# Kernel optimization log

Hardware: AMD Instinct MI355X
Metric: run time of the kernel (lower is better)

The kernel has to match this reference:

```python
import jax, jax.numpy as jnp
import numpy as np

HIDDEN = 1024
EMB = 256
VOCAB = 500000
B = 4096
C = 128
EPS = 1e-12


def setup_inputs() -> dict:
    key = jax.random.key(0)
    ks = jax.random.split(key, 8)
    hidden_states = jax.random.normal(ks[0], (B, HIDDEN), dtype=jnp.float32)
    cand_idx = jax.random.randint(ks[1], (B, C), 0, VOCAB, dtype=jnp.int32)
    W_dense = jax.random.normal(ks[2], (EMB, HIDDEN), dtype=jnp.float32) * (1.0 / np.sqrt(HIDDEN))
    b_dense = jnp.zeros((EMB,), dtype=jnp.float32)
    ln_gamma = jnp.ones((EMB,), dtype=jnp.float32)
    ln_beta = jnp.zeros((EMB,), dtype=jnp.float32)
    decoder_table = jax.random.normal(ks[3], (VOCAB, EMB), dtype=jnp.float32) * 0.02
    entity_bias = jnp.zeros((VOCAB,), dtype=jnp.float32)
    return {
        "hidden_states": hidden_states,
        "W_dense": W_dense,
        "b_dense": b_dense,
        "ln_gamma": ln_gamma,
        "ln_beta": ln_beta,
        "decoder_table": decoder_table,
        "entity_bias": entity_bias,
        "cand_idx": cand_idx,
    }


def _transform(x, W_dense, b_dense, ln_gamma, ln_beta):
    # Linear hidden_size -> entity_emb_size, gelu, LayerNorm
    h = x @ W_dense.T + b_dense
    h = jax.nn.gelu(h, approximate=False)
    mu = jnp.mean(h, axis=-1, keepdims=True)
    var = jnp.mean(jnp.square(h - mu), axis=-1, keepdims=True)
    return (h - mu) * jax.lax.rsqrt(var + EPS) * ln_gamma + ln_beta


def reference(hidden_states, W_dense, b_dense, ln_gamma, ln_beta, decoder_table, entity_bias, cand_idx):
    h = _transform(hidden_states, W_dense, b_dense, ln_gamma, ln_beta)  # [B, EMB]
    cand_emb = decoder_table[cand_idx]          # [B, C, EMB] ragged gather (padded)
    bias = entity_bias[cand_idx]                # [B, C]
    scores = jnp.einsum('bce,be->bc', cand_emb, h) + bias  # [B, C]
    return scores
```

## Files before the change

### kernel.cpp

```cpp
#include <hip/hip_runtime.h>
#include <hip/hip_bf16.h>
#include <math.h>

#define HIDDEN 1024
#define EMB    256
#define BROWS  4096
#define CAND   128
#define LN_EPS 1e-12f

typedef __attribute__((ext_vector_type(8))) short bf16x8;
typedef __attribute__((ext_vector_type(4))) float f32x4;

__device__ __forceinline__ int swz(int row, int slot) { return slot ^ ((row >> 1) & 3); }

__device__ __forceinline__ unsigned short f2bf(float f) {
    __bf16 h = (__bf16)f;
    return __builtin_bit_cast(unsigned short, h);
}

__device__ __forceinline__ float gelu(float x) {
    return 0.5f * x * (1.0f + erff(x * 0.70710678118654752f));
}

__global__ __launch_bounds__(256) void k_gemm_partial(
    const float* __restrict__ A,
    const float* __restrict__ W,
    float* __restrict__ P)
{
    __shared__ unsigned short As[16 * 32];
    __shared__ unsigned short Ws[256 * 32];

    const int tid  = threadIdx.x;
    const int lane = tid & 63;
    const int wv   = tid >> 6;
    const int m0   = blockIdx.x * 16;
    const int ks   = blockIdx.y;
    const int kbeg = ks * 256;

    const int lcol = lane & 15;
    const int lk   = lane >> 4;
    const int arow = tid >> 2, apr = tid & 3;

    float4 a0, a1, w0[4], w1[4];

#define LOADREGS(KT)                                                          \
    if (tid < 64) {                                                           \
        a0 = *(const float4*)&A[(size_t)(m0 + arow) * HIDDEN + (KT) + apr * 8];     \
        a1 = *(const float4*)&A[(size_t)(m0 + arow) * HIDDEN + (KT) + apr * 8 + 4]; \
    }                                                                         \
    _Pragma("unroll")                                                         \
    for (int i = 0; i < 4; ++i) {                                             \
        int id = tid + i * 256;                                               \
        int row = id >> 2, pr = id & 3;                                       \
        w0[i] = *(const float4*)&W[(size_t)row * HIDDEN + (KT) + pr * 8];     \
        w1[i] = *(const float4*)&W[(size_t)row * HIDDEN + (KT) + pr * 8 + 4]; \
    }

    f32x4 acc[4] = {};
    LOADREGS(kbeg)

    for (int it = 0; it < 8; ++it) {
        __syncthreads();
        if (tid < 64) {
            bf16x8 v;
            v[0]=f2bf(a0.x); v[1]=f2bf(a0.y); v[2]=f2bf(a0.z); v[3]=f2bf(a0.w);
            v[4]=f2bf(a1.x); v[5]=f2bf(a1.y); v[6]=f2bf(a1.z); v[7]=f2bf(a1.w);
            *(bf16x8*)&As[arow * 32 + swz(arow, apr) * 8] = v;
        }
        #pragma unroll
        for (int i = 0; i < 4; ++i) {
            int id = tid + i * 256;
            int row = id >> 2, pr = id & 3;
            bf16x8 v;
            v[0]=f2bf(w0[i].x); v[1]=f2bf(w0[i].y); v[2]=f2bf(w0[i].z); v[3]=f2bf(w0[i].w);
            v[4]=f2bf(w1[i].x); v[5]=f2bf(w1[i].y); v[6]=f2bf(w1[i].z); v[7]=f2bf(w1[i].w);
            *(bf16x8*)&Ws[row * 32 + swz(row, pr) * 8] = v;
        }
        __syncthreads();
        if (it < 7) { LOADREGS(kbeg + (it + 1) * 32) }
        bf16x8 af = *(const bf16x8*)&As[lcol * 32 + swz(lcol, lk) * 8];
        bf16x8 bfr[4];
        #pragma unroll
        for (int n = 0; n < 4; ++n) {
            int r = wv * 64 + n * 16 + lcol;
            bfr[n] = *(const bf16x8*)&Ws[r * 32 + swz(r, lk) * 8];
        }
        #pragma unroll
        for (int n = 0; n < 4; ++n)
            acc[n] = __builtin_amdgcn_mfma_f32_16x16x32_bf16(af, bfr[n], acc[n], 0, 0, 0);
    }
#undef LOADREGS

    float* Pout = P + (size_t)ks * ((size_t)BROWS * EMB);
    #pragma unroll
    for (int n = 0; n < 4; ++n)
        #pragma unroll
        for (int r = 0; r < 4; ++r) {
            int R   = lk * 4 + r;
            int col = wv * 64 + n * 16 + lcol;
            Pout[(size_t)(m0 + R) * EMB + col] = acc[n][r];
        }
}

__global__ __launch_bounds__(256) void k_finalize(
    const float* __restrict__ P,
    const float* __restrict__ bias,
    const float* __restrict__ gamma,
    const float* __restrict__ beta,
    float* __restrict__ G)
{
    const int tid  = threadIdx.x;
    const int lane = tid & 63;
    const int row  = blockIdx.x * 4 + (tid >> 6);
    const size_t off = (size_t)row * EMB + lane * 4;
    const size_t S   = (size_t)BROWS * EMB;

    float4 v0 = *(const float4*)&P[off];
    float4 v1 = *(const float4*)&P[off + S];
    float4 v2 = *(const float4*)&P[off + 2 * S];
    float4 v3 = *(const float4*)&P[off + 3 * S];
    float4 bb = *(const float4*)&bias[lane * 4];

    float4 h;
    h.x = gelu(v0.x + v1.x + v2.x + v3.x + bb.x);
    h.y = gelu(v0.y + v1.y + v2.y + v3.y + bb.y);
    h.z = gelu(v0.z + v1.z + v2.z + v3.z + bb.z);
    h.w = gelu(v0.w + v1.w + v2.w + v3.w + bb.w);

    float s = h.x + h.y + h.z + h.w;
    #pragma unroll
    for (int m = 32; m >= 1; m >>= 1) s += __shfl_xor(s, m);
    const float mu = s * (1.0f / 256.0f);

    const float dx = h.x - mu, dy = h.y - mu, dz = h.z - mu, dw = h.w - mu;
    float q = dx * dx + dy * dy + dz * dz + dw * dw;
    #pragma unroll
    for (int m = 32; m >= 1; m >>= 1) q += __shfl_xor(q, m);
    const float rs = rsqrtf(q * (1.0f / 256.0f) + LN_EPS);

    float4 g  = *(const float4*)&gamma[lane * 4];
    float4 be = *(const float4*)&beta[lane * 4];
    float4 o;
    o.x = dx * rs * g.x + be.x;
    o.y = dy * rs * g.y + be.y;
    o.z = dz * rs * g.z + be.z;
    o.w = dw * rs * g.w + be.w;
    *(float4*)&G[off] = o;
}

__global__ __launch_bounds__(256) void k_scores(
    const float* __restrict__ H,
    const float* __restrict__ table,
    const float* __restrict__ ebias,
    const int*   __restrict__ cidx,
    float* __restrict__ out)
{
    __shared__ float smem[16384];
    const int tid  = threadIdx.x;
    const int lane = tid & 63;
    const int wv   = tid >> 6;
    const int l    = lane & 15;
    const int q    = lane >> 4;
    const int b     = blockIdx.x >> 1;
    const int cbase = (blockIdx.x & 1) * 64 + wv * 16;

    const float4* Hrow = (const float4*)(H + (size_t)b * EMB);
    float4 hv[4];
    #pragma unroll
    for (int p = 0; p < 4; ++p) hv[p] = Hrow[p * 16 + l];

    const int sidxv = cidx[(size_t)b * CAND + cbase + l];
    const float ebv = ebias[sidxv];

    float* wbase = &smem[wv * 4096];
    #pragma unroll
    for (int r = 0; r < 16; ++r) {
        int idx = __shfl(sidxv, r);
        const float* gsrc = table + (size_t)idx * EMB + lane * 4;
        __builtin_amdgcn_global_load_lds(
            (const __attribute__((address_space(1))) void*)gsrc,
            (__attribute__((address_space(3))) void*)(wbase + r * 256),
            16, 0, 0);
    }

    float res[4];
#define DOGROUP(g, WN)                                                        \
    {                                                                         \
        asm volatile("s_waitcnt vmcnt(" WN ")" ::: "memory");                 \
        const float4* row = (const float4*)(wbase + (4 * (g) + q) * 256);     \
        float s = 0.f;                                                        \
        _Pragma("unroll")                                                     \
        for (int p = 0; p < 4; ++p) {                                         \
            float4 t = row[p * 16 + l];                                       \
            s += t.x * hv[p].x + t.y * hv[p].y + t.z * hv[p].z + t.w * hv[p].w;\
        }                                                                     \
        _Pragma("unroll")                                                     \
        for (int m = 8; m >= 1; m >>= 1) s += __shfl_xor(s, m);               \
        res[g] = s;                                                           \
    }
    DOGROUP(0, "12")
    DOGROUP(1, "8")
    DOGROUP(2, "4")
    DOGROUP(3, "0")
#undef DOGROUP

    #pragma unroll
    for (int g = 0; g < 4; ++g) {
        float eb = __shfl(ebv, 4 * g + q);
        if (l == 0) out[(size_t)b * CAND + cbase + 4 * g + q] = res[g] + eb;
    }
}

extern "C" void kernel_launch(void* const* d_in, const int* in_sizes, int n_in,
                              void* d_out, int out_size, void* d_ws, size_t ws_size,
                              hipStream_t stream) {
    const float* hidden = (const float*)d_in[0];
    const float* Wd     = (const float*)d_in[1];
    const float* bd     = (const float*)d_in[2];
    const float* gamma  = (const float*)d_in[3];
    const float* beta   = (const float*)d_in[4];
    const float* table  = (const float*)d_in[5];
    const float* ebias  = (const float*)d_in[6];
    const int*   cidx   = (const int*)d_in[7];
    float* out = (float*)d_out;

    char* ws = (char*)d_ws;
    float* G = (float*)ws;
    float* P = (float*)(ws + 4 * 1024 * 1024);

    k_gemm_partial<<<dim3(BROWS / 16, 4), 256, 0, stream>>>(hidden, Wd, P);
    k_finalize<<<dim3(BROWS / 4), 256, 0, stream>>>(P, bd, gamma, beta, G);
    k_scores<<<dim3(BROWS * 2), 256, 0, stream>>>(G, table, ebias, cidx, out);
}
```

Measured before the change: 119.7 us.

## Make scores kernel persistent with double-buffered LDS gather prefetch

The scores kernel previously launched one short-lived block per half row. It now launches 512 persistent blocks, and each wave walks 32 chunks of 8 candidates. While the current chunk is being computed, the wave prefetches the next chunk's table rows into a second LDS buffer, along with its H row, candidate indices and bias. The goal is to hide gather latency and remove per-block launch and prologue overhead. The cost is in-flight parallelism that is fixed by the grid size, plus more complex vmcnt bookkeeping.

```diff
diff --git a/kernel.cpp b/kernel.cpp
--- a/kernel.cpp
+++ b/kernel.cpp
@@ -7,6 +7,10 @@
 #define BROWS  4096
 #define CAND   128
 #define LN_EPS 1e-12f
+
+#define NC     8
+#define NWTOT  2048
+#define NITER  32
 
 typedef __attribute__((ext_vector_type(8))) short bf16x8;
 typedef __attribute__((ext_vector_type(4))) float f32x4;
@@ -149,7 +153,7 @@
 }
 
 __global__ __launch_bounds__(256) void k_scores(
-    const float* __restrict__ H,
+    const float* __restrict__ Hf,
     const float* __restrict__ table,
     const float* __restrict__ ebias,
     const int*   __restrict__ cidx,
@@ -161,54 +165,99 @@
     const int wv   = tid >> 6;
     const int l    = lane & 15;
     const int q    = lane >> 4;
-    const int b     = blockIdx.x >> 1;
-    const int cbase = (blockIdx.x & 1) * 64 + wv * 16;
-
-    const float4* Hrow = (const float4*)(H + (size_t)b * EMB);
-    float4 hv[4];
-    #pragma unroll
-    for (int p = 0; p < 4; ++p) hv[p] = Hrow[p * 16 + l];
-
-    const int sidxv = cidx[(size_t)b * CAND + cbase + l];
-    const float ebv = ebias[sidxv];
-
-    float* wbase = &smem[wv * 4096];
-    #pragma unroll
-    for (int r = 0; r < 16; ++r) {
-        int idx = __shfl(sidxv, r);
-        const float* gsrc = table + (size_t)idx * EMB + lane * 4;
+    const int w    = blockIdx.x * 4 + wv;
+
+    float* buf0 = &smem[wv * 4096];
+    float* buf1 = buf0 + 2048;
+
+#define CH(IT) ((((IT) < NITER) ? (IT) : (NITER - 1)) * NWTOT + w)
+
+    int ia = cidx[(size_t)CH(0) * NC + (l & 7)];
+    int ib = cidx[(size_t)CH(1) * NC + (l & 7)];
+    float4 ha[4];
+    {
+        const float4* Hr = (const float4*)(Hf + (size_t)(CH(0) >> 4) * EMB);
+        #pragma unroll
+        for (int p = 0; p < 4; ++p) ha[p] = Hr[p * 16 + l];
+    }
+    float ea = ebias[ia];
+    #pragma unroll
+    for (int r = 0; r < NC; ++r) {
+        int ix = __shfl(ia, r);
+        const float* gs = table + (size_t)ix * EMB + lane * 4;
         __builtin_amdgcn_global_load_lds(
-            (const __attribute__((address_space(1))) void*)gsrc,
-            (__attribute__((address_space(3))) void*)(wbase + r * 256),
+            (const __attribute__((address_space(1))) void*)gs,
+            (__attribute__((address_space(3))) void*)(buf0 + r * 256),
             16, 0, 0);
     }
 
-    float res[4];
-#define DOGROUP(g, WN)                                                        \
-    {                                                                         \
-        asm volatile("s_waitcnt vmcnt(" WN ")" ::: "memory");                 \
-        const float4* row = (const float4*)(wbase + (4 * (g) + q) * 256);     \
-        float s = 0.f;                                                        \
-        _Pragma("unroll")                                                     \
-        for (int p = 0; p < 4; ++p) {                                         \
-            float4 t = row[p * 16 + l];                                       \
-            s += t.x * hv[p].x + t.y * hv[p].y + t.z * hv[p].z + t.w * hv[p].w;\
-        }                                                                     \
-        _Pragma("unroll")                                                     \
-        for (int m = 8; m >= 1; m >>= 1) s += __shfl_xor(s, m);               \
-        res[g] = s;                                                           \
-    }
-    DOGROUP(0, "12")
-    DOGROUP(1, "8")
-    DOGROUP(2, "4")
-    DOGROUP(3, "0")
-#undef DOGROUP
-
-    #pragma unroll
-    for (int g = 0; g < 4; ++g) {
-        float eb = __shfl(ebv, 4 * g + q);
-        if (l == 0) out[(size_t)b * CAND + cbase + 4 * g + q] = res[g] + eb;
-    }
+    #pragma unroll 2
+    for (int it = 0; it < NITER; ++it) {
+        float* bcur = (it & 1) ? buf1 : buf0;
+        float* bnxt = (it & 1) ? buf0 : buf1;
+
+        int ic = cidx[(size_t)CH(it + 2) * NC + (l & 7)];
+        float4 hn[4];
+        {
+            const float4* Hr = (const float4*)(Hf + (size_t)(CH(it + 1) >> 4) * EMB);
+            #pragma unroll
+            for (int p = 0; p < 4; ++p) hn[p] = Hr[p * 16 + l];
+        }
+        float en = ebias[ib];
+        #pragma unroll
+        for (int r = 0; r < NC; ++r) {
+            int ix = __shfl(ib, r);
+            const float* gs = table + (size_t)ix * EMB + lane * 4;
+            __builtin_amdgcn_global_load_lds(
+                (const __attribute__((address_space(1))) void*)gs,
+                (__attribute__((address_space(3))) void*)(bnxt + r * 256),
+                16, 0, 0);
+        }
+
+        float res0, res1;
+        asm volatile("s_waitcnt vmcnt(12)" ::: "memory");
+        {
+            const float4* row = (const float4*)(bcur + q * 256);
+            float s = 0.f;
+            #pragma unroll
+            for (int p = 0; p < 4; ++p) {
+                float4 t = row[p * 16 + l];
+                s += t.x * ha[p].x + t.y * ha[p].y + t.z * ha[p].z + t.w * ha[p].w;
+            }
+            #pragma unroll
+            for (int m = 8; m >= 1; m >>= 1) s += __shfl_xor(s, m);
+            res0 = s;
+        }
+        asm volatile("s_waitcnt vmcnt(8)" ::: "memory");
+        {
+            const float4* row = (const float4*)(bcur + (4 + q) * 256);
+            float s = 0.f;
+            #pragma unroll
+            for (int p = 0; p < 4; ++p) {
+                float4 t = row[p * 16 + l];
+                s += t.x * ha[p].x + t.y * ha[p].y + t.z * ha[p].z + t.w * ha[p].w;
+            }
+            #pragma unroll
+            for (int m = 8; m >= 1; m >>= 1) s += __shfl_xor(s, m);
+            res1 = s;
+        }
+
+        {
+            const size_t obase = (size_t)CH(it) * NC;
+            float e0 = __shfl(ea, q);
+            float e1 = __shfl(ea, 4 + q);
+            if (l == 0) {
+                out[obase + q]     = res0 + e0;
+                out[obase + 4 + q] = res1 + e1;
+            }
+        }
+
+        ia = ib; ib = ic;
+        ea = en;
+        #pragma unroll
+        for (int p = 0; p < 4; ++p) ha[p] = hn[p];
+    }
+#undef CH
 }
 
 extern "C" void kernel_launch(void* const* d_in, const int* in_sizes, int n_in,
@@ -230,5 +279,5 @@
 
     k_gemm_partial<<<dim3(BROWS / 16, 4), 256, 0, stream>>>(hidden, Wd, P);
     k_finalize<<<dim3(BROWS / 4), 256, 0, stream>>>(P, bd, gamma, beta, G);
-    k_scores<<<dim3(BROWS * 2), 256, 0, stream>>>(G, table, ebias, cidx, out);
-}
+    k_scores<<<dim3(512), 256, 0, stream>>>(G, table, ebias, cidx, out);
+}
```

Result: no change. 120.5 us (+0.7%).

## Bucket-sort candidate indices by table row to localize embedding gathers

Applied to the files above, without the earlier changes.

Adds a counting sort (zero, histogram, scan, scatter kernels) that groups all B*C candidate entries into 1024 buckets by vocabulary index. The scoring kernel then walks entries in bucket order and swizzles block IDs across buckets, so concurrently running blocks fetch table rows from nearby address ranges, improving cache and TLB locality. Each wave now reloads the transformed hidden row per group of four entries and scatters outputs to arbitrary positions. The cost is four extra launches, an 8 MB entry buffer written and read back, and scattered output writes.

```diff
diff --git a/kernel.cpp b/kernel.cpp
--- a/kernel.cpp
+++ b/kernel.cpp
@@ -8,6 +8,12 @@
 #define CAND   128
 #define LN_EPS 1e-12f
 
+#define NENT   (BROWS * CAND)
+#define NB     1024
+#define BKT_SH 9
+
+typedef unsigned int u32;
+typedef unsigned long long u64;
 typedef __attribute__((ext_vector_type(8))) short bf16x8;
 typedef __attribute__((ext_vector_type(4))) float f32x4;
 
@@ -148,44 +154,129 @@
     *(float4*)&G[off] = o;
 }
 
-__global__ __launch_bounds__(256) void k_scores(
-    const float* __restrict__ H,
+__global__ __launch_bounds__(256) void k_zero(u32* __restrict__ bkt_pad)
+{
+    bkt_pad[blockIdx.x * 256 + threadIdx.x] = 0;
+}
+
+__global__ __launch_bounds__(256) void k_count(
+    const int* __restrict__ cidx, u32* __restrict__ bkt_pad)
+{
+    __shared__ u32 lh[NB];
+    const int tid = threadIdx.x;
+    for (int t = tid; t < NB; t += 256) lh[t] = 0;
+    __syncthreads();
+    const int base = blockIdx.x * 8192;
+    #pragma unroll
+    for (int i = 0; i < 32; ++i) {
+        int idx = cidx[base + i * 256 + tid];
+        atomicAdd(&lh[idx >> BKT_SH], 1u);
+    }
+    __syncthreads();
+    for (int t = tid; t < NB; t += 256) {
+        u32 v = lh[t];
+        if (v) atomicAdd(&bkt_pad[t * 16], v);
+    }
+}
+
+__global__ __launch_bounds__(1024) void k_scan(u32* __restrict__ bkt_pad)
+{
+    __shared__ u32 a[NB];
+    const int t = threadIdx.x;
+    const u32 own = bkt_pad[t * 16];
+    a[t] = own;
+    __syncthreads();
+    for (int off = 1; off < NB; off <<= 1) {
+        u32 add = (t >= off) ? a[t - off] : 0u;
+        __syncthreads();
+        a[t] += add;
+        __syncthreads();
+    }
+    bkt_pad[t * 16] = a[t] - own;
+}
+
+__global__ __launch_bounds__(256) void k_scatter(
+    const int* __restrict__ cidx, u32* __restrict__ bkt_pad,
+    u64* __restrict__ ent)
+{
+    __shared__ u32 lh[NB];
+    __shared__ u32 lb[NB];
+    __shared__ u32 lo[NB];
+    const int tid = threadIdx.x;
+    for (int t = tid; t < NB; t += 256) { lh[t] = 0; lo[t] = 0; }
+    __syncthreads();
+    const int base = blockIdx.x * 8192;
+    u32 iv[32];
+    #pragma unroll
+    for (int i = 0; i < 32; ++i) {
+        iv[i] = (u32)cidx[base + i * 256 + tid];
+        atomicAdd(&lh[iv[i] >> BKT_SH], 1u);
+    }
+    __syncthreads();
+    for (int t = tid; t < NB; t += 256) {
+        u32 v = lh[t];
+        if (v) lb[t] = atomicAdd(&bkt_pad[t * 16], v);
+    }
+    __syncthreads();
+    #pragma unroll
+    for (int i = 0; i < 32; ++i) {
+        u32 bkt = iv[i] >> BKT_SH;
+        u32 p = lb[bkt] + atomicAdd(&lo[bkt], 1u);
+        ent[p] = ((u64)(u32)(base + i * 256 + tid) << 32) | iv[i];
+    }
+}
+
+__global__ __launch_bounds__(256) void k_gather(
+    const float* __restrict__ G,
     const float* __restrict__ table,
     const float* __restrict__ ebias,
-    const int*   __restrict__ cidx,
+    const u64*  __restrict__ ent,
     float* __restrict__ out)
 {
     __shared__ float smem[16384];
+    const int bid  = blockIdx.x;
+    const int work = (bid & 7) * 1024 + (bid >> 3);
     const int tid  = threadIdx.x;
     const int lane = tid & 63;
     const int wv   = tid >> 6;
     const int l    = lane & 15;
     const int q    = lane >> 4;
-    const int b     = blockIdx.x >> 1;
-    const int cbase = (blockIdx.x & 1) * 64 + wv * 16;
-
-    const float4* Hrow = (const float4*)(H + (size_t)b * EMB);
-    float4 hv[4];
-    #pragma unroll
-    for (int p = 0; p < 4; ++p) hv[p] = Hrow[p * 16 + l];
-
-    const int sidxv = cidx[(size_t)b * CAND + cbase + l];
-    const float ebv = ebias[sidxv];
+
+    const int gbase = work * 64 + wv * 16;
+
+    const u64 pk  = ent[gbase + l];
+    const int idxv = (int)(pk & 0xffffffffu);
+    const int ev   = (int)(pk >> 32);
+    const float ebv = ebias[idxv];
 
     float* wbase = &smem[wv * 4096];
     #pragma unroll
     for (int r = 0; r < 16; ++r) {
-        int idx = __shfl(sidxv, r);
-        const float* gsrc = table + (size_t)idx * EMB + lane * 4;
+        int ix = __shfl(idxv, r);
+        const float* gsrc = table + (size_t)ix * EMB + lane * 4;
         __builtin_amdgcn_global_load_lds(
             (const __attribute__((address_space(1))) void*)gsrc,
             (__attribute__((address_space(3))) void*)(wbase + r * 256),
             16, 0, 0);
     }
 
-    float res[4];
+    float4 hv[4];
+    {
+        int e0 = __shfl(ev, q);
+        const float4* Hr = (const float4*)(G + (size_t)(e0 >> 7) * EMB);
+        #pragma unroll
+        for (int p = 0; p < 4; ++p) hv[p] = Hr[p * 16 + l];
+    }
+
 #define DOGROUP(g, WN)                                                        \
     {                                                                         \
+        float4 hn[4];                                                         \
+        if ((g) < 3) {                                                        \
+            int en_ = __shfl(ev, 4 * ((g) + 1) + q);                          \
+            const float4* Hr = (const float4*)(G + (size_t)(en_ >> 7) * EMB); \
+            _Pragma("unroll")                                                 \
+            for (int p = 0; p < 4; ++p) hn[p] = Hr[p * 16 + l];               \
+        }                                                                     \
         asm volatile("s_waitcnt vmcnt(" WN ")" ::: "memory");                 \
         const float4* row = (const float4*)(wbase + (4 * (g) + q) * 256);     \
         float s = 0.f;                                                        \
@@ -196,19 +287,19 @@
         }                                                                     \
         _Pragma("unroll")                                                     \
         for (int m = 8; m >= 1; m >>= 1) s += __shfl_xor(s, m);               \
-        res[g] = s;                                                           \
+        float eb = __shfl(ebv, 4 * (g) + q);                                  \
+        int   eo = __shfl(ev,  4 * (g) + q);                                  \
+        if (l == 0) out[eo] = s + eb;                                         \
+        if ((g) < 3) {                                                        \
+            _Pragma("unroll")                                                 \
+            for (int p = 0; p < 4; ++p) hv[p] = hn[p];                        \
+        }                                                                     \
     }
     DOGROUP(0, "12")
     DOGROUP(1, "8")
     DOGROUP(2, "4")
     DOGROUP(3, "0")
 #undef DOGROUP
-
-    #pragma unroll
-    for (int g = 0; g < 4; ++g) {
-        float eb = __shfl(ebv, 4 * g + q);
-        if (l == 0) out[(size_t)b * CAND + cbase + 4 * g + q] = res[g] + eb;
-    }
 }
 
 extern "C" void kernel_launch(void* const* d_in, const int* in_sizes, int n_in,
@@ -225,10 +316,18 @@
     float* out = (float*)d_out;
 
     char* ws = (char*)d_ws;
-    float* G = (float*)ws;
-    float* P = (float*)(ws + 4 * 1024 * 1024);
+    float* G       = (float*)ws;
+    float* P       = (float*)(ws + (4u << 20));
+    u32*   bkt_pad = (u32*)(ws + (20u << 20));
+    u64*   ent     = (u64*)(ws + (20u << 20) + (64u << 10));
+
+    k_zero   <<<dim3(64), 256, 0, stream>>>(bkt_pad);
+    k_count  <<<dim3(64), 256, 0, stream>>>(cidx, bkt_pad);
+    k_scan   <<<dim3(1), 1024, 0, stream>>>(bkt_pad);
+    k_scatter<<<dim3(64), 256, 0, stream>>>(cidx, bkt_pad, ent);
 
     k_gemm_partial<<<dim3(BROWS / 16, 4), 256, 0, stream>>>(hidden, Wd, P);
     k_finalize<<<dim3(BROWS / 4), 256, 0, stream>>>(P, bd, gamma, beta, G);
-    k_scores<<<dim3(BROWS * 2), 256, 0, stream>>>(G, table, ebias, cidx, out);
-}
+
+    k_gather<<<dim3(NENT / 64), 256, 0, stream>>>(G, table, ebias, ent, out);
+}
```

After: 172.6 us. 44.2% more time.
